# Kernel optimization log

Measured on AMD Instinct MI355X. Metric: run time of the kernel, lower is better.

Reference implementation:

```python
import jax, jax.numpy as jnp
import numpy as np

WS = 7          # window size (square)
HEADS = 16
LOGIT_MAX = float(np.log(1.0 / 0.01))


def _consts():
    # Continuous relative position bias coordinate table, Swin-v2 log-spaced.
    r = np.arange(-(WS - 1), WS)
    table = np.stack(np.meshgrid(r, r, indexing='ij'), axis=-1).astype(np.float32)  # [2W-1, 2W-1, 2]
    table = table / (WS - 1) * 8.0
    table = np.sign(table) * np.log2(np.abs(table) + 1.0) / np.log2(8.0)
    # Relative position index [N, N] into the flattened table.
    coords = np.stack(np.meshgrid(np.arange(WS), np.arange(WS), indexing='ij')).reshape(2, -1)
    rel = coords[:, :, None] - coords[:, None, :]
    idx = (rel[0] + WS - 1) * (2 * WS - 1) + (rel[1] + WS - 1)  # [49, 49]
    return table.reshape(-1, 2), idx.astype(np.int32)


def setup_inputs() -> dict:
    key = jax.random.key(0)
    ks = jax.random.split(key, 6)
    B, N, C = 2048, WS * WS, 512
    d = C // HEADS
    return {
        'x': jax.random.normal(ks[0], (B, N, C), jnp.float32),
        'w_qkv': jax.random.normal(ks[1], (C, 3 * C), jnp.float32) * (C ** -0.5),
        'q_bias': jnp.zeros((C,), jnp.float32),
        'v_bias': jnp.zeros((C,), jnp.float32),
        'logit_scale': jnp.full((HEADS, 1, 1), np.log(10.0), jnp.float32),
        'cpb_w1': jax.random.normal(ks[2], (2, 512), jnp.float32) * (2 ** -0.5),
        'cpb_b1': jnp.zeros((512,), jnp.float32),
        'cpb_w2': jax.random.normal(ks[3], (512, HEADS), jnp.float32) * (512 ** -0.5),
        'proj_w': jax.random.normal(ks[4], (C, C), jnp.float32) * (C ** -0.5),
        'proj_b': jnp.zeros((C,), jnp.float32),
    }


def _l2norm(x):
    # matches tf.math.l2_normalize (eps=1e-12 under a max)
    return x / jnp.sqrt(jnp.maximum(jnp.sum(x * x, axis=-1, keepdims=True), 1e-12))


def reference(x, w_qkv, q_bias, v_bias, logit_scale, cpb_w1, cpb_b1, cpb_w2, proj_w, proj_b):
    table, idx = _consts()
    table = jnp.asarray(table)   # [(2W-1)^2, 2]
    idx = jnp.asarray(idx)       # [N, N] int32 (constant)

    B, N, C = x.shape
    d = C // HEADS

    qkv = (x @ w_qkv).reshape(B, N, 3, HEADS, d).transpose(2, 0, 3, 1, 4)  # [3, B, H, N, d]
    q, k, v = qkv[0], qkv[1], qkv[2]
    q = q + q_bias.reshape(HEADS, 1, d)
    v = v + v_bias.reshape(HEADS, 1, d)

    # cosine attention with clamped learned logit scale
    attn = jnp.einsum('bhnd,bhmd->bhnm', _l2norm(q), _l2norm(k))
    scale = jnp.exp(jnp.minimum(logit_scale, LOGIT_MAX))  # [H,1,1]
    attn = attn * scale[None]

    # CPB MLP -> gather -> sigmoid bias
    bias_table = jax.nn.relu(table @ cpb_w1 + cpb_b1) @ cpb_w2          # [(2W-1)^2, H]
    bias = bias_table[idx.reshape(-1)].reshape(N, N, HEADS).transpose(2, 0, 1)  # [H, N, N]
    bias = 16.0 * jax.nn.sigmoid(bias)

    attn = jax.nn.softmax(attn + bias[None], axis=-1)

    out = jnp.einsum('bhnm,bhmd->bhnd', attn, v).transpose(0, 2, 1, 3).reshape(B, N, C)
    return out @ proj_w + proj_b
```

## Files before the change

### kernel.cpp

```cpp
#include <hip/hip_runtime.h>
#include <hip/hip_bf16.h>

typedef __bf16 bf16;
typedef __attribute__((ext_vector_type(8))) __bf16 bf16x8;
typedef __attribute__((ext_vector_type(4))) __bf16 bf16x4;
typedef __attribute__((ext_vector_type(4))) float floatx4;

#define HEADS 16
#define NTOK 49
#define MROWS (2048 * 49)
#define LOGIT_MAX 4.6051702f


__device__ __forceinline__ void gload16(const void* g, void* l) {
  __builtin_amdgcn_global_load_lds((const __attribute__((address_space(1))) void*)g,
                                   (__attribute__((address_space(3))) void*)l, 16, 0, 0);
}


__global__ void cvt_x(const float* __restrict__ in, bf16* __restrict__ out, int n4) {
  int i = blockIdx.x * blockDim.x + threadIdx.x;
  const int stride = gridDim.x * blockDim.x;
  for (; i < n4; i += stride) {
    float4 v = ((const float4*)in)[i];
    bf16x4 o;
    o[0] = (bf16)v.x; o[1] = (bf16)v.y; o[2] = (bf16)v.z; o[3] = (bf16)v.w;
    *(bf16x4*)&out[(long)i * 4] = o;
  }
}

__global__ void transpose_bf16(const float* __restrict__ in, bf16* __restrict__ out,
                               int R, int C) {
  int idx = blockIdx.x * blockDim.x + threadIdx.x;
  if (idx < R * C) {
    int r = idx / C, c = idx % C;
    out[(long)c * R + r] = (bf16)in[(long)r * C + c];
  }
}


__global__ void cpb_mlp(const float* __restrict__ w1, const float* __restrict__ b1,
                        const float* __restrict__ w2, float* __restrict__ out169) {
  const int r = blockIdx.x;
  const int ti = r / 13, tj = r % 13;
  float v0 = (float)(ti - 6) * (8.0f / 6.0f);
  float v1 = (float)(tj - 6) * (8.0f / 6.0f);
  float s0 = (v0 > 0.f) ? 1.f : ((v0 < 0.f) ? -1.f : 0.f);
  float s1 = (v1 > 0.f) ? 1.f : ((v1 < 0.f) ? -1.f : 0.f);
  const float t0 = s0 * log2f(fabsf(v0) + 1.0f) * (1.0f / 3.0f);
  const float t1 = s1 * log2f(fabsf(v1) + 1.0f) * (1.0f / 3.0f);

  float acc[16];
#pragma unroll
  for (int h = 0; h < 16; ++h) acc[h] = 0.f;

  for (int c = threadIdx.x; c < 512; c += 64) {
    float hv = fmaxf(t0 * w1[c] + t1 * w1[512 + c] + b1[c], 0.f);
#pragma unroll
    for (int h = 0; h < 16; ++h) acc[h] += hv * w2[c * 16 + h];
  }
#pragma unroll
  for (int h = 0; h < 16; ++h) {
    float s = acc[h];
    for (int off = 32; off > 0; off >>= 1) s += __shfl_down(s, off);
    if (threadIdx.x == 0) out169[r * 16 + h] = s;
  }
}

__global__ void bias_expand(const float* __restrict__ out169, float* __restrict__ bias_sig) {
  int idx = blockIdx.x * blockDim.x + threadIdx.x;
  if (idx < 16 * 64 * 52) {
    int h = idx / 3328;
    int rem = idx % 3328;
    int q = rem / 52, k = rem % 52;
    float val = 0.f;
    if (q < 49 && k < 49) {
      int di = q / 7 - k / 7 + 6;
      int dj = q % 7 - k % 7 + 6;
      float v = out169[(di * 13 + dj) * 16 + h];
      val = 16.0f / (1.0f + expf(-v));
    }
    bias_sig[idx] = val;
  }
}


__device__ __forceinline__ void stage_half(const bf16* __restrict__ G, int ldg,
                                           bf16* lds, int half, int w, int lane) {
#pragma unroll
  for (int j = 0; j < 2; ++j) {
    const int rr = (w * 2 + j) * 8;
    const int row = half * 128 + rr + (lane >> 3);
    const int slot = (lane & 7) ^ (lane >> 3);
    gload16(G + (long)row * ldg + slot * 8, lds + (half * 128 + rr) * 64);
  }
}

#define BAR() __builtin_amdgcn_s_barrier()
#define WAITDS() asm volatile("s_waitcnt lgkmcnt(0)" ::: "memory")
#define WAITVM(N) asm volatile("s_waitcnt vmcnt(" #N ")" ::: "memory")

#define LOAD_A(MQ, BUF) do { \
  _Pragma("unroll") for (int m_ = 0; m_ < 4; ++m_) \
  _Pragma("unroll") for (int t_ = 0; t_ < 2; ++t_) { \
    const int row_ = wm * 128 + (MQ) * 64 + m_ * 16 + l15; \
    const int s_ = t_ * 4 + g; \
    af[m_][t_] = *(const bf16x8*)&AS[BUF][row_][(s_ ^ (row_ & 7)) * 8]; \
  } } while (0)

#define LOAD_B(NQ, BUF) do { \
  _Pragma("unroll") for (int n_ = 0; n_ < 2; ++n_) \
  _Pragma("unroll") for (int t_ = 0; t_ < 2; ++t_) { \
    const int row_ = wn * 64 + (NQ) * 32 + n_ * 16 + l15; \
    const int s_ = t_ * 4 + g; \
    bfr[NQ][n_][t_] = *(const bf16x8*)&BS[BUF][row_][(s_ ^ (row_ & 7)) * 8]; \
  } } while (0)

#define MFMA_Q(MQ, NQ) do { \
  __builtin_amdgcn_s_setprio(1); \
  _Pragma("unroll") for (int t_ = 0; t_ < 2; ++t_) \
  _Pragma("unroll") for (int m_ = 0; m_ < 4; ++m_) \
  _Pragma("unroll") for (int n_ = 0; n_ < 2; ++n_) \
    acc[(MQ) * 4 + m_][(NQ) * 2 + n_] = __builtin_amdgcn_mfma_f32_16x16x32_bf16( \
        af[m_][t_], bfr[NQ][n_][t_], acc[(MQ) * 4 + m_][(NQ) * 2 + n_], 0, 0, 0); \
  __builtin_amdgcn_s_setprio(0); \
} while (0)

template <int EPI>
__global__ __launch_bounds__(512, 2)
void gemm256(const bf16* __restrict__ A, const bf16* __restrict__ BT,
             void* __restrict__ Cout, const float* __restrict__ bias0,
             const float* __restrict__ bias1, int NT, int K, long N) {
  __shared__ bf16 AS[2][256][64];
  __shared__ bf16 BS[2][256][64];
  const int tid = threadIdx.x;
  const int lane = tid & 63, w = tid >> 6;
  const int l15 = lane & 15, g = lane >> 4;
  const int wm = w >> 2, wn = w & 3;

  int wg = blockIdx.x;
  wg = (wg & 7) * (gridDim.x >> 3) + (wg >> 3);
  const long m0 = (long)(wg / NT) * 256;
  const long n0 = (long)(wg % NT) * 256;

  const bf16* Ab = A + m0 * K;
  const bf16* Bb = BT + n0 * K;

  floatx4 acc[8][4] = {};
  bf16x8 af[4][2], bfr[2][2][2];

  stage_half(Ab, K, &AS[0][0][0], 0, w, lane);
  stage_half(Ab, K, &AS[0][0][0], 1, w, lane);
  stage_half(Bb, K, &BS[0][0][0], 0, w, lane);
  stage_half(Bb, K, &BS[0][0][0], 1, w, lane);
  stage_half(Bb + 64, K, &BS[1][0][0], 0, w, lane);
  stage_half(Bb + 64, K, &BS[1][0][0], 1, w, lane);
  WAITVM(4);
  BAR();

  const int NI = K >> 7;
  for (int i = 0; i < NI - 1; ++i) {
    const int t1 = 2 * i + 1, t2 = 2 * i + 2, t3 = 2 * i + 3;
    LOAD_A(0, 0); LOAD_B(0, 0);
    stage_half(Ab + t1 * 64, K, &AS[1][0][0], 0, w, lane);
    BAR(); WAITDS(); MFMA_Q(0, 0); BAR();
    LOAD_B(1, 0);
    stage_half(Ab + t1 * 64, K, &AS[1][0][0], 1, w, lane);
    BAR(); WAITDS(); MFMA_Q(0, 1); BAR();
    LOAD_A(1, 0);
    stage_half(Bb + t2 * 64, K, &BS[0][0][0], 0, w, lane);
    BAR(); WAITDS(); MFMA_Q(1, 0); BAR();
    stage_half(Bb + t2 * 64, K, &BS[0][0][0], 1, w, lane);
    WAITVM(4);
    BAR(); MFMA_Q(1, 1); BAR();
    LOAD_A(0, 1); LOAD_B(0, 1);
    stage_half(Ab + t2 * 64, K, &AS[0][0][0], 0, w, lane);
    BAR(); WAITDS(); MFMA_Q(0, 0); BAR();
    LOAD_B(1, 1);
    stage_half(Ab + t2 * 64, K, &AS[0][0][0], 1, w, lane);
    BAR(); WAITDS(); MFMA_Q(0, 1); BAR();
    LOAD_A(1, 1);
    stage_half(Bb + t3 * 64, K, &BS[1][0][0], 0, w, lane);
    BAR(); WAITDS(); MFMA_Q(1, 0); BAR();
    stage_half(Bb + t3 * 64, K, &BS[1][0][0], 1, w, lane);
    WAITVM(4);
    BAR(); MFMA_Q(1, 1); BAR();
  }
  {
    const int t1 = 2 * NI - 1;
    LOAD_A(0, 0); LOAD_B(0, 0);
    stage_half(Ab + t1 * 64, K, &AS[1][0][0], 0, w, lane);
    BAR(); WAITDS(); MFMA_Q(0, 0); BAR();
    LOAD_B(1, 0);
    stage_half(Ab + t1 * 64, K, &AS[1][0][0], 1, w, lane);
    BAR(); WAITDS(); MFMA_Q(0, 1); BAR();
    LOAD_A(1, 0);
    BAR(); WAITDS(); MFMA_Q(1, 0); BAR();
    WAITVM(0);
    BAR(); MFMA_Q(1, 1); BAR();
    LOAD_A(0, 1); LOAD_B(0, 1);
    BAR(); WAITDS(); MFMA_Q(0, 0); BAR();
    LOAD_B(1, 1);
    BAR(); WAITDS(); MFMA_Q(0, 1); BAR();
    LOAD_A(1, 1);
    BAR(); WAITDS(); MFMA_Q(1, 0); BAR();
    WAITDS(); MFMA_Q(1, 1);
  }

#pragma unroll
  for (int m = 0; m < 8; ++m) {
#pragma unroll
    for (int n = 0; n < 4; ++n) {
      const long col = n0 + wn * 64 + n * 16 + l15;
      float badd;
      if (EPI == 0)
        badd = (col < 512) ? bias0[col] : ((col >= 1024) ? bias1[col - 1024] : 0.0f);
      else
        badd = bias0[col];
#pragma unroll
      for (int r = 0; r < 4; ++r) {
        const long row = m0 + wm * 128 + m * 16 + g * 4 + r;
        const float v = acc[m][n][r] + badd;
        if (EPI == 0)
          ((bf16*)Cout)[row * N + col] = (bf16)v;
        else
          ((float*)Cout)[row * N + col] = v;
      }
    }
  }
}


__global__ __launch_bounds__(256)
void attn_mfma(const bf16* __restrict__ qkv, const float* __restrict__ bias_sig,
               const float* __restrict__ logit_scale, bf16* __restrict__ aout) {
  __shared__ __align__(16) bf16 Plds[4][16 * 72];
  const int tid = threadIdx.x;
  const int wave = tid >> 6, lane = tid & 63;
  const int l15 = lane & 15, g = lane >> 4;
  const int bh = blockIdx.x * 4 + wave;
  const int b = bh >> 4, h = bh & 15;
  const long base = (long)b * NTOK * 1536 + h * 32;
  const bf16* Qg = qkv + base;
  const bf16* Kg = qkv + base + 512;
  const bf16* Vg = qkv + base + 1024;
  bf16* P = Plds[wave];

  const float scale = __expf(fminf(logit_scale[h], LOGIT_MAX));

  bf16x8 kf[4];
#pragma unroll
  for (int kt = 0; kt < 4; ++kt) {
    const int row = kt * 16 + l15;
    bf16x8 raw = *(const bf16x8*)(Kg + (long)row * 1536 + g * 8);
    float fv[8], ss = 0.f;
#pragma unroll
    for (int j = 0; j < 8; ++j) { fv[j] = (float)raw[j]; ss += fv[j] * fv[j]; }
    ss += __shfl_xor(ss, 16);
    ss += __shfl_xor(ss, 32);
    const float rk = rsqrtf(fmaxf(ss, 1e-12f));
#pragma unroll
    for (int j = 0; j < 8; ++j) kf[kt][j] = (bf16)(fv[j] * rk);
  }

  bf16x8 vf[2][2];
#pragma unroll
  for (int dt = 0; dt < 2; ++dt)
#pragma unroll
    for (int t = 0; t < 2; ++t)
#pragma unroll
      for (int i = 0; i < 8; ++i) {
        const int k = t * 32 + g * 8 + i;
        vf[dt][t][i] = (k < NTOK) ? Vg[(long)k * 1536 + dt * 16 + l15] : (bf16)0.0f;
      }

  const floatx4 zero = {};
  const int swz = l15 & 3;

  for (int qt = 0; qt < 4; ++qt) {
    const int qrow = qt * 16 + l15;
    bf16x8 qraw = *(const bf16x8*)(Qg + (long)qrow * 1536 + g * 8);
    float fq[8], ssq = 0.f;
#pragma unroll
    for (int j = 0; j < 8; ++j) { fq[j] = (float)qraw[j]; ssq += fq[j] * fq[j]; }
    ssq += __shfl_xor(ssq, 16);
    ssq += __shfl_xor(ssq, 32);
    const float rq = rsqrtf(fmaxf(ssq, 1e-12f));
    bf16x8 qf;
#pragma unroll
    for (int j = 0; j < 8; ++j) qf[j] = (bf16)(fq[j] * rq);

    float4 b4[4];
#pragma unroll
    for (int kt = 0; kt < 4; ++kt)
      b4[kt] = *(const float4*)(bias_sig + h * 3328 + qrow * 52 + kt * 16 + g * 4);

    floatx4 st[4];
#pragma unroll
    for (int kt = 0; kt < 4; ++kt)
      st[kt] = __builtin_amdgcn_mfma_f32_16x16x32_bf16(kf[kt], qf, zero, 0, 0, 0);

    float sv[4][4];
    float m = -1e30f;
#pragma unroll
    for (int kt = 0; kt < 4; ++kt)
#pragma unroll
      for (int r = 0; r < 4; ++r) {
        const int k = kt * 16 + g * 4 + r;
        const float s = (k < NTOK) ? st[kt][r] * scale + ((const float*)&b4[kt])[r] : -1e30f;
        sv[kt][r] = s;
        m = fmaxf(m, s);
      }
    m = fmaxf(m, __shfl_xor(m, 16));
    m = fmaxf(m, __shfl_xor(m, 32));
    float l = 0.f;
#pragma unroll
    for (int kt = 0; kt < 4; ++kt)
#pragma unroll
      for (int r = 0; r < 4; ++r) {
        const float p = __expf(sv[kt][r] - m);
        sv[kt][r] = p;
        l += p;
      }
    l += __shfl_xor(l, 16);
    l += __shfl_xor(l, 32);
    const float inv = 1.0f / l;

#pragma unroll
    for (int kt = 0; kt < 4; ++kt) {
      bf16x4 pk;
#pragma unroll
      for (int r = 0; r < 4; ++r) pk[r] = (bf16)(sv[kt][r] * inv);
      *(bf16x4*)&P[l15 * 72 + (kt ^ swz) * 16 + g * 4] = pk;
    }
    bf16x8 ap[2];
#pragma unroll
    for (int t = 0; t < 2; ++t) {
      const int gran = (2 * t + (g >> 1)) ^ swz;
      ap[t] = *(const bf16x8*)&P[l15 * 72 + gran * 16 + (g & 1) * 8];
    }

    floatx4 ot[2] = {};
#pragma unroll
    for (int dt = 0; dt < 2; ++dt)
#pragma unroll
      for (int t = 0; t < 2; ++t)
        ot[dt] = __builtin_amdgcn_mfma_f32_16x16x32_bf16(ap[t], vf[dt][t], ot[dt], 0, 0, 0);

#pragma unroll
    for (int dt = 0; dt < 2; ++dt)
#pragma unroll
      for (int r = 0; r < 4; ++r) {
        const int qg2 = qt * 16 + g * 4 + r;
        if (qg2 < NTOK)
          aout[(long)b * NTOK * 512 + (long)qg2 * 512 + h * 32 + dt * 16 + l15] =
              (bf16)ot[dt][r];
      }
  }
}


extern "C" void kernel_launch(void* const* d_in, const int* in_sizes, int n_in,
                              void* d_out, int out_size, void* d_ws, size_t ws_size,
                              hipStream_t stream) {
  (void)in_sizes; (void)n_in; (void)out_size; (void)ws_size;
  const float* x           = (const float*)d_in[0];
  const float* w_qkv       = (const float*)d_in[1];
  const float* q_bias      = (const float*)d_in[2];
  const float* v_bias      = (const float*)d_in[3];
  const float* logit_scale = (const float*)d_in[4];
  const float* cpb_w1      = (const float*)d_in[5];
  const float* cpb_b1      = (const float*)d_in[6];
  const float* cpb_w2      = (const float*)d_in[7];
  const float* proj_w      = (const float*)d_in[8];
  const float* proj_b      = (const float*)d_in[9];
  float* out = (float*)d_out;

  char* ws = (char*)d_ws;
  const size_t QKV_B  = 308281344;
  const size_t XBF_B  = 102760448;
  const size_t WQT_B  = 1572864;
  const size_t PJT_B  = 524288;
  const size_t T169_B = 10816;
  bf16*  qkv      = (bf16*)ws;
  bf16*  xbf      = (bf16*)(ws + QKV_B);
  bf16*  wqkvT    = (bf16*)(ws + QKV_B + XBF_B);
  bf16*  projT    = (bf16*)(ws + QKV_B + XBF_B + WQT_B);
  float* tab169   = (float*)(ws + QKV_B + XBF_B + WQT_B + PJT_B);
  float* bias_sig = (float*)(ws + QKV_B + XBF_B + WQT_B + PJT_B + T169_B);

  cvt_x<<<2048, 256, 0, stream>>>(x, xbf, MROWS * 512 / 4);
  transpose_bf16<<<3072, 256, 0, stream>>>(w_qkv, wqkvT, 512, 1536);
  transpose_bf16<<<1024, 256, 0, stream>>>(proj_w, projT, 512, 512);
  cpb_mlp<<<169, 64, 0, stream>>>(cpb_w1, cpb_b1, cpb_w2, tab169);
  bias_expand<<<208, 256, 0, stream>>>(tab169, bias_sig);

  gemm256<0><<<392 * 6, 512, 0, stream>>>(xbf, wqkvT, qkv, q_bias, v_bias,
                                          6, 512, 1536);
  attn_mfma<<<8192, 256, 0, stream>>>(qkv, bias_sig, logit_scale, xbf);
  gemm256<1><<<392 * 2, 512, 0, stream>>>(xbf, projT, out, proj_b, nullptr,
                                          2, 512, 512);
}
```

Before: 599.6 us.

## Write QKV head-major from GEMM epilogue and keep softmax probabilities in registers

Measured after the change: 674.7 us. 1.13x slower.

```diff
diff --git a/kernel.cpp b/kernel.cpp
--- a/kernel.cpp
+++ b/kernel.cpp
@@ -9,6 +9,7 @@
 #define HEADS 16
 #define NTOK 49
 #define MROWS (2048 * 49)
+#define TILE_E 1568
 #define LOGIT_MAX 4.6051702f
 
 
@@ -16,6 +17,10 @@
   __builtin_amdgcn_global_load_lds((const __attribute__((address_space(1))) void*)g,
                                    (__attribute__((address_space(3))) void*)l, 16, 0, 0);
 }
+
+#define BAR() __builtin_amdgcn_s_barrier()
+#define WAITDS() asm volatile("s_waitcnt lgkmcnt(0)" ::: "memory")
+#define WAITVM(N) asm volatile("s_waitcnt vmcnt(" #N ")" ::: "memory")
 
 
 __global__ void cvt_x(const float* __restrict__ in, bf16* __restrict__ out, int n4) {
@@ -96,10 +101,6 @@
   }
 }
 
-#define BAR() __builtin_amdgcn_s_barrier()
-#define WAITDS() asm volatile("s_waitcnt lgkmcnt(0)" ::: "memory")
-#define WAITVM(N) asm volatile("s_waitcnt vmcnt(" #N ")" ::: "memory")
-
 #define LOAD_A(MQ, BUF) do { \
   _Pragma("unroll") for (int m_ = 0; m_ < 4; ++m_) \
   _Pragma("unroll") for (int t_ = 0; t_ < 2; ++t_) { \
@@ -130,7 +131,9 @@
 __global__ __launch_bounds__(512, 2)
 void gemm256(const bf16* __restrict__ A, const bf16* __restrict__ BT,
              void* __restrict__ Cout, const float* __restrict__ bias0,
-             const float* __restrict__ bias1, int NT, int K, long N) {
+             const float* __restrict__ bias1,
+             bf16* __restrict__ Qp, bf16* __restrict__ Kp, bf16* __restrict__ Vp,
+             int NT, int K, long N) {
   __shared__ bf16 AS[2][256][64];
   __shared__ bf16 BS[2][256][64];
   const int tid = threadIdx.x;
@@ -207,44 +210,65 @@
     WAITDS(); MFMA_Q(1, 1);
   }
 
-#pragma unroll
-  for (int m = 0; m < 8; ++m) {
-#pragma unroll
-    for (int n = 0; n < 4; ++n) {
-      const long col = n0 + wn * 64 + n * 16 + l15;
-      float badd;
-      if (EPI == 0)
-        badd = (col < 512) ? bias0[col] : ((col >= 1024) ? bias1[col - 1024] : 0.0f);
-      else
-        badd = bias0[col];
+  if (EPI == 0) {
+#pragma unroll
+    for (int m = 0; m < 8; ++m) {
 #pragma unroll
       for (int r = 0; r < 4; ++r) {
-        const long row = m0 + wm * 128 + m * 16 + g * 4 + r;
-        const float v = acc[m][n][r] + badd;
-        if (EPI == 0)
-          ((bf16*)Cout)[row * N + col] = (bf16)v;
-        else
-          ((float*)Cout)[row * N + col] = v;
+        const int row = (int)m0 + wm * 128 + m * 16 + g * 4 + r;
+        const int b = row / 49;
+        const int nr = row - b * 49;
+        const long rb = (long)b * 16 * TILE_E + (long)nr * 32;
+#pragma unroll
+        for (int n = 0; n < 4; ++n) {
+          const int col = (int)n0 + wn * 64 + n * 16 + l15;
+          const int mat = col >> 9;
+          const int hh = (col >> 5) & 15;
+          const int d = col & 31;
+          bf16* dst = (mat == 0) ? Qp : ((mat == 1) ? Kp : Vp);
+          const float badd = (mat == 0) ? bias0[col]
+                            : ((mat == 2) ? bias1[col - 1024] : 0.0f);
+          dst[rb + (long)hh * TILE_E + d] = (bf16)(acc[m][n][r] + badd);
+        }
       }
     }
+  } else {
+#pragma unroll
+    for (int m = 0; m < 8; ++m) {
+#pragma unroll
+      for (int n = 0; n < 4; ++n) {
+        const long col = n0 + wn * 64 + n * 16 + l15;
+        const float badd = bias0[col];
+#pragma unroll
+        for (int r = 0; r < 4; ++r) {
+          const long row = m0 + wm * 128 + m * 16 + g * 4 + r;
+          ((float*)Cout)[row * N + col] = acc[m][n][r] + badd;
+        }
+      }
+    }
   }
 }
 
 
 __global__ __launch_bounds__(256)
-void attn_mfma(const bf16* __restrict__ qkv, const float* __restrict__ bias_sig,
+void attn_mfma(const bf16* __restrict__ Qa, const bf16* __restrict__ Ka,
+               const bf16* __restrict__ Va, const float* __restrict__ bias_sig,
                const float* __restrict__ logit_scale, bf16* __restrict__ aout) {
-  __shared__ __align__(16) bf16 Plds[4][16 * 72];
+  __shared__ __align__(16) bf16 Vlds[4][2048];
   const int tid = threadIdx.x;
   const int wave = tid >> 6, lane = tid & 63;
   const int l15 = lane & 15, g = lane >> 4;
   const int bh = blockIdx.x * 4 + wave;
-  const int b = bh >> 4, h = bh & 15;
-  const long base = (long)b * NTOK * 1536 + h * 32;
-  const bf16* Qg = qkv + base;
-  const bf16* Kg = qkv + base + 512;
-  const bf16* Vg = qkv + base + 1024;
-  bf16* P = Plds[wave];
+  const int h = bh & 15;
+  const long tbase = (long)bh * TILE_E;
+  const bf16* Qt = Qa + tbase;
+  const bf16* Kt = Ka + tbase;
+  const bf16* Vt = Va + tbase;
+  bf16* VL = Vlds[wave];
+
+#pragma unroll
+  for (int j = 0; j < 4; ++j)
+    gload16(Vt + j * 512 + lane * 8, VL + j * 512);
 
   const float scale = __expf(fminf(logit_scale[h], LOGIT_MAX));
 
@@ -252,7 +276,7 @@
 #pragma unroll
   for (int kt = 0; kt < 4; ++kt) {
     const int row = kt * 16 + l15;
-    bf16x8 raw = *(const bf16x8*)(Kg + (long)row * 1536 + g * 8);
+    bf16x8 raw = *(const bf16x8*)(Kt + row * 32 + g * 8);
     float fv[8], ss = 0.f;
 #pragma unroll
     for (int j = 0; j < 8; ++j) { fv[j] = (float)raw[j]; ss += fv[j] * fv[j]; }
@@ -263,6 +287,8 @@
     for (int j = 0; j < 8; ++j) kf[kt][j] = (bf16)(fv[j] * rk);
   }
 
+  asm volatile("s_waitcnt vmcnt(0)" ::: "memory");
+  __builtin_amdgcn_sched_barrier(0);
   bf16x8 vf[2][2];
 #pragma unroll
   for (int dt = 0; dt < 2; ++dt)
@@ -270,16 +296,15 @@
     for (int t = 0; t < 2; ++t)
 #pragma unroll
       for (int i = 0; i < 8; ++i) {
-        const int k = t * 32 + g * 8 + i;
-        vf[dt][t][i] = (k < NTOK) ? Vg[(long)k * 1536 + dt * 16 + l15] : (bf16)0.0f;
+        const int kk = t * 32 + (i >> 2) * 16 + g * 4 + (i & 3);
+        vf[dt][t][i] = VL[kk * 32 + dt * 16 + l15];
       }
 
   const floatx4 zero = {};
-  const int swz = l15 & 3;
 
   for (int qt = 0; qt < 4; ++qt) {
     const int qrow = qt * 16 + l15;
-    bf16x8 qraw = *(const bf16x8*)(Qg + (long)qrow * 1536 + g * 8);
+    bf16x8 qraw = *(const bf16x8*)(Qt + qrow * 32 + g * 8);
     float fq[8], ssq = 0.f;
 #pragma unroll
     for (int j = 0; j < 8; ++j) { fq[j] = (float)qraw[j]; ssq += fq[j] * fq[j]; }
@@ -326,26 +351,19 @@
     l += __shfl_xor(l, 32);
     const float inv = 1.0f / l;
 
-#pragma unroll
-    for (int kt = 0; kt < 4; ++kt) {
-      bf16x4 pk;
-#pragma unroll
-      for (int r = 0; r < 4; ++r) pk[r] = (bf16)(sv[kt][r] * inv);
-      *(bf16x4*)&P[l15 * 72 + (kt ^ swz) * 16 + g * 4] = pk;
-    }
-    bf16x8 ap[2];
-#pragma unroll
-    for (int t = 0; t < 2; ++t) {
-      const int gran = (2 * t + (g >> 1)) ^ swz;
-      ap[t] = *(const bf16x8*)&P[l15 * 72 + gran * 16 + (g & 1) * 8];
-    }
+    bf16x8 pa[2];
+#pragma unroll
+    for (int t = 0; t < 2; ++t)
+#pragma unroll
+      for (int i = 0; i < 8; ++i)
+        pa[t][i] = (bf16)(sv[2 * t + (i >> 2)][i & 3] * inv);
 
     floatx4 ot[2] = {};
 #pragma unroll
     for (int dt = 0; dt < 2; ++dt)
 #pragma unroll
       for (int t = 0; t < 2; ++t)
-        ot[dt] = __builtin_amdgcn_mfma_f32_16x16x32_bf16(ap[t], vf[dt][t], ot[dt], 0, 0, 0);
+        ot[dt] = __builtin_amdgcn_mfma_f32_16x16x32_bf16(pa[t], vf[dt][t], ot[dt], 0, 0, 0);
 
 #pragma unroll
     for (int dt = 0; dt < 2; ++dt)
@@ -353,7 +371,7 @@
       for (int r = 0; r < 4; ++r) {
         const int qg2 = qt * 16 + g * 4 + r;
         if (qg2 < NTOK)
-          aout[(long)b * NTOK * 512 + (long)qg2 * 512 + h * 32 + dt * 16 + l15] =
+          aout[((long)(bh >> 4) * NTOK + qg2) * 512 + h * 32 + dt * 16 + l15] =
               (bf16)ot[dt][r];
       }
   }
@@ -377,17 +395,18 @@
   float* out = (float*)d_out;
 
   char* ws = (char*)d_ws;
-  const size_t QKV_B  = 308281344;
-  const size_t XBF_B  = 102760448;
+  const size_t ARR_B  = 102760448;
   const size_t WQT_B  = 1572864;
   const size_t PJT_B  = 524288;
   const size_t T169_B = 10816;
-  bf16*  qkv      = (bf16*)ws;
-  bf16*  xbf      = (bf16*)(ws + QKV_B);
-  bf16*  wqkvT    = (bf16*)(ws + QKV_B + XBF_B);
-  bf16*  projT    = (bf16*)(ws + QKV_B + XBF_B + WQT_B);
-  float* tab169   = (float*)(ws + QKV_B + XBF_B + WQT_B + PJT_B);
-  float* bias_sig = (float*)(ws + QKV_B + XBF_B + WQT_B + PJT_B + T169_B);
+  bf16*  Qa       = (bf16*)ws;
+  bf16*  Ka       = (bf16*)(ws + ARR_B);
+  bf16*  Va       = (bf16*)(ws + 2 * ARR_B);
+  bf16*  xbf      = (bf16*)(ws + 3 * ARR_B);
+  bf16*  wqkvT    = (bf16*)(ws + 4 * ARR_B);
+  bf16*  projT    = (bf16*)(ws + 4 * ARR_B + WQT_B);
+  float* tab169   = (float*)(ws + 4 * ARR_B + WQT_B + PJT_B);
+  float* bias_sig = (float*)(ws + 4 * ARR_B + WQT_B + PJT_B + T169_B);
 
   cvt_x<<<2048, 256, 0, stream>>>(x, xbf, MROWS * 512 / 4);
   transpose_bf16<<<3072, 256, 0, stream>>>(w_qkv, wqkvT, 512, 1536);
@@ -395,9 +414,9 @@
   cpb_mlp<<<169, 64, 0, stream>>>(cpb_w1, cpb_b1, cpb_w2, tab169);
   bias_expand<<<208, 256, 0, stream>>>(tab169, bias_sig);
 
-  gemm256<0><<<392 * 6, 512, 0, stream>>>(xbf, wqkvT, qkv, q_bias, v_bias,
-                                          6, 512, 1536);
-  attn_mfma<<<8192, 256, 0, stream>>>(qkv, bias_sig, logit_scale, xbf);
+  gemm256<0><<<392 * 6, 512, 0, stream>>>(xbf, wqkvT, nullptr, q_bias, v_bias,
+                                          Qa, Ka, Va, 6, 512, 1536);
+  attn_mfma<<<8192, 256, 0, stream>>>(Qa, Ka, Va, bias_sig, logit_scale, xbf);
   gemm256<1><<<392 * 2, 512, 0, stream>>>(xbf, projT, out, proj_b, nullptr,
-                                          2, 512, 512);
-}
+                                          nullptr, nullptr, nullptr, 2, 512, 512);
+}
```
